# Performance work log

Hardware: AMD Instinct MI355X
Metric: run time of the kernel (lower is better)

Reference implementation:

```python
import jax, jax.numpy as jnp
import numpy as np

# Sizes (match input_specs)
B = 50                 # number of CRN graphs in the batch
NS_PER, NR_PER = 2000, 4000
N_S, N_R = B * NS_PER, B * NR_PER   # 100k species, 200k reactions total
E = 1_000_000          # bipartite edges
D = 128                # d_model
L = 2                  # n_layers
N_TYPES, P_DIM = 16, 8
MAX_SPECIES_IDX = 2000


def setup_inputs() -> dict:
    key = jax.random.key(0)
    ks = jax.random.split(key, 12)
    inp = {
        "species_indices": jax.random.randint(ks[0], (N_S,), 0, MAX_SPECIES_IDX, dtype=jnp.int32),
        "is_external": jax.random.randint(ks[1], (N_S,), 0, 2, dtype=jnp.int32),
        "propensity_type_ids": jax.random.randint(ks[2], (N_R,), 0, N_TYPES, dtype=jnp.int32),
        "propensity_params": jax.random.normal(ks[3], (N_R, P_DIM), dtype=jnp.float32),
        "edge_species": jax.random.randint(ks[4], (E,), 0, N_S, dtype=jnp.int32),
        "edge_reaction": jax.random.randint(ks[5], (E,), 0, N_R, dtype=jnp.int32),
        # contiguous per-graph segment ids (graphs are equal-sized)
        "species_batch": jnp.repeat(jnp.arange(B, dtype=jnp.int32), NS_PER),
        "reaction_batch": jnp.repeat(jnp.arange(B, dtype=jnp.int32), NR_PER),
        # learned parameters
        "species_table": jax.random.normal(ks[6], (MAX_SPECIES_IDX, D), dtype=jnp.float32) * 0.02,
        "external_table": jax.random.normal(ks[7], (2, D), dtype=jnp.float32) * 0.02,
        "type_table": jax.random.normal(ks[8], (N_TYPES, D), dtype=jnp.float32) * 0.02,
        "W_param": jax.random.normal(ks[9], (P_DIM, D), dtype=jnp.float32) * 0.1,
        "b_param": jnp.zeros((D,), dtype=jnp.float32),
        # per-layer message-passing weights: concat([h, msg]) -> d
        "Wr": jax.random.normal(ks[10], (L, 2 * D, D), dtype=jnp.float32) * 0.05,
        "br": jnp.zeros((L, D), dtype=jnp.float32),
        "Ws": jax.random.normal(ks[11], (L, 2 * D, D), dtype=jnp.float32) * 0.05,
        "bs": jnp.zeros((L, D), dtype=jnp.float32),
    }
    return inp


def reference(species_indices, is_external, propensity_type_ids, propensity_params,
              edge_species, edge_reaction, species_batch, reaction_batch,
              species_table, external_table, type_table, W_param, b_param,
              Wr, br, Ws, bs):
    # Initial embeddings
    h_s = species_table[species_indices] + external_table[is_external]          # (N_S, D)
    h_r = type_table[propensity_type_ids] + propensity_params @ W_param + b_param  # (N_R, D)

    n_s, n_r = h_s.shape[0], h_r.shape[0]
    # Alternating bipartite sum message passing (SumMessagePassingLayer)
    for l in range(Wr.shape[0]):
        m_r = jax.ops.segment_sum(h_s[edge_species], edge_reaction, num_segments=n_r)
        h_r = jax.nn.relu(jnp.concatenate([h_r, m_r], axis=-1) @ Wr[l] + br[l])
        m_s = jax.ops.segment_sum(h_r[edge_reaction], edge_species, num_segments=n_s)
        h_s = jax.nn.relu(jnp.concatenate([h_s, m_s], axis=-1) @ Ws[l] + bs[l])

    # Segment-mean pooling per graph (index_add then divide by counts)
    pooled_s = jax.ops.segment_sum(h_s, species_batch, num_segments=B) / float(NS_PER)
    pooled_r = jax.ops.segment_sum(h_r, reaction_batch, num_segments=B) / float(NR_PER)
    context = jnp.concatenate([pooled_s, pooled_r], axis=-1)  # (B, 2D); dropout p=0 -> identity
    return context
```

## Files before the change

### kernel.cpp

```cpp
#include <hip/hip_runtime.h>
#include <stdint.h>

#define NS 100000
#define NR 200000
#define EE 1000000
#define DD 128
#define NB 50
#define NSP 2000
#define NRP 4000
#define BSH 10
#define NBR 196
#define NBS 98
#define CHUNK 8192

typedef short bf16x8 __attribute__((ext_vector_type(8)));
typedef float f32x4 __attribute__((ext_vector_type(4)));
typedef unsigned u32x4 __attribute__((ext_vector_type(4)));
typedef unsigned u32x2 __attribute__((ext_vector_type(2)));

__device__ __forceinline__ unsigned short f2bf(float f){
  unsigned u = __float_as_uint(f);
  u = (u + 0x7FFFu + ((u >> 16) & 1u)) >> 16;
  return (unsigned short)u;
}
__device__ __forceinline__ float bf2f(unsigned short s){
  return __uint_as_float(((unsigned)s) << 16);
}
__device__ __forceinline__ unsigned packbf(float a, float b){
  return (unsigned)f2bf(a) | ((unsigned)f2bf(b) << 16);
}
__device__ __forceinline__ float bflo(unsigned p){ return __uint_as_float(p << 16); }
__device__ __forceinline__ float bfhi(unsigned p){ return __uint_as_float(p & 0xFFFF0000u); }

__global__ void pack_w(const float* __restrict__ Wr, const float* __restrict__ Ws,
                       unsigned short* __restrict__ Wp){
  int g = blockIdx.x*256 + threadIdx.x;
  if (g >= 4*32768) return;
  int j = g & 7; int rest = g >> 3;
  int lane = rest & 63; rest >>= 6;
  int ks = rest & 7; rest >>= 3;
  int ct = rest & 7; int mat = rest >> 3;
  int k  = ks*32 + (lane >> 4)*8 + j;
  int cc = ct*16 + (lane & 15);
  const float* src = (mat < 2) ? (Wr + (size_t)mat*256*DD) : (Ws + (size_t)(mat-2)*256*DD);
  Wp[g] = f2bf(src[(size_t)k*DD + cc]);
}

__global__ __launch_bounds__(256) void init_all(const int* __restrict__ si, const int* __restrict__ ext,
        const int* __restrict__ tid, const float* __restrict__ pp,
        const float* __restrict__ st, const float* __restrict__ et, const float* __restrict__ tt,
        const float* __restrict__ Wpar, const float* __restrict__ bpar,
        unsigned short* __restrict__ hs, unsigned short* __restrict__ hr){
  int g = blockIdx.x*256 + threadIdx.x;
  int row = g >> 4, colb = (g & 15) * 8;
  if (row < NS){
    const float* a = st + (size_t)si[row]*DD + colb;
    const float* b = et + (size_t)ext[row]*DD + colb;
    float4 x0 = ((const float4*)a)[0], x1 = ((const float4*)a)[1];
    float4 y0 = ((const float4*)b)[0], y1 = ((const float4*)b)[1];
    u32x4 o;
    o.x = packbf(x0.x+y0.x, x0.y+y0.y);
    o.y = packbf(x0.z+y0.z, x0.w+y0.w);
    o.z = packbf(x1.x+y1.x, x1.y+y1.y);
    o.w = packbf(x1.z+y1.z, x1.w+y1.w);
    *(u32x4*)(hs + (size_t)row*DD + colb) = o;
  } else {
    int r = row - NS;
    const float* tb = tt + (size_t)tid[r]*DD + colb;
    float4 a0 = ((const float4*)tb)[0], a1 = ((const float4*)tb)[1];
    float4 b0 = ((const float4*)(bpar+colb))[0], b1 = ((const float4*)(bpar+colb))[1];
    a0.x += b0.x; a0.y += b0.y; a0.z += b0.z; a0.w += b0.w;
    a1.x += b1.x; a1.y += b1.y; a1.z += b1.z; a1.w += b1.w;
    const float* pr = pp + (size_t)r*8;
    float4 p0 = ((const float4*)pr)[0], p1 = ((const float4*)pr)[1];
    float w[8] = {p0.x,p0.y,p0.z,p0.w,p1.x,p1.y,p1.z,p1.w};
    #pragma unroll
    for (int p = 0; p < 8; p++){
      float4 w0 = ((const float4*)(Wpar + p*DD + colb))[0];
      float4 w1 = ((const float4*)(Wpar + p*DD + colb))[1];
      a0.x += w[p]*w0.x; a0.y += w[p]*w0.y; a0.z += w[p]*w0.z; a0.w += w[p]*w0.w;
      a1.x += w[p]*w1.x; a1.y += w[p]*w1.y; a1.z += w[p]*w1.z; a1.w += w[p]*w1.w;
    }
    u32x4 o;
    o.x = packbf(a0.x, a0.y); o.y = packbf(a0.z, a0.w);
    o.z = packbf(a1.x, a1.y); o.w = packbf(a1.z, a1.w);
    *(u32x4*)(hr + (size_t)r*DD + colb) = o;
  }
}

__global__ __launch_bounds__(256) void bucket_hist(const int* __restrict__ er, const int* __restrict__ es,
                                                   int* __restrict__ gcnt){
  __shared__ int cnt[NBR + NBS];
  int t = threadIdx.x;
  for (int j = t; j < NBR + NBS; j += 256) cnt[j] = 0;
  __syncthreads();
  long i0 = (long)blockIdx.x * 2048;
  for (int j = t; j < 2048; j += 256){
    long i = i0 + j;
    if (i < EE){
      atomicAdd(&cnt[er[i] >> BSH], 1);
      atomicAdd(&cnt[NBR + (es[i] >> BSH)], 1);
    }
  }
  __syncthreads();
  for (int j = t; j < NBR + NBS; j += 256)
    if (cnt[j]) atomicAdd(&gcnt[j], cnt[j]);
}

__global__ __launch_bounds__(256) void bucket_scan(const int* __restrict__ gcnt,
        int* __restrict__ bktOffR, int* __restrict__ bktOffS,
        int* __restrict__ gCurR, int* __restrict__ gCurS){
  __shared__ int a[256];
  int t = threadIdx.x;
  int own = (t < NBR) ? gcnt[t] : 0;
  a[t] = own; __syncthreads();
  for (int d = 1; d < 256; d <<= 1){
    int x = (t >= d) ? a[t-d] : 0;
    __syncthreads(); a[t] += x; __syncthreads();
  }
  if (t < NBR){ int v = a[t] - own; bktOffR[t] = v; gCurR[t] = v; }
  if (t == 0) bktOffR[NBR] = EE;
  __syncthreads();
  own = (t < NBS) ? gcnt[NBR + t] : 0;
  a[t] = own; __syncthreads();
  for (int d = 1; d < 256; d <<= 1){
    int x = (t >= d) ? a[t-d] : 0;
    __syncthreads(); a[t] += x; __syncthreads();
  }
  if (t < NBS){ int v = a[t] - own; bktOffS[t] = v; gCurS[t] = v; }
  if (t == 0) bktOffS[NBS] = EE;
}

__global__ __launch_bounds__(256) void bin_edges(const int* __restrict__ er, const int* __restrict__ es,
        int* __restrict__ gCurR, int* __restrict__ gCurS,
        unsigned* __restrict__ recR, unsigned* __restrict__ recS){
  __shared__ unsigned stage[CHUNK];
  __shared__ unsigned char stageb[CHUNK];
  __shared__ int cnt[256], scn[256], pref[256], gbase[256], lcur[256];
  int t = threadIdx.x;
  int side = blockIdx.y;
  const int* dest = side ? es : er;
  const int* srca = side ? er : es;
  int* gCur = side ? gCurS : gCurR;
  unsigned* rec = side ? recS : recR;
  int nbkt = side ? NBS : NBR;
  long i0 = (long)blockIdx.x * CHUNK;
  int n = (EE - i0 < CHUNK) ? (int)(EE - i0) : CHUNK;
  cnt[t] = 0;
  __syncthreads();
  for (int j = t; j < n; j += 256)
    atomicAdd(&cnt[dest[i0 + j] >> BSH], 1);
  __syncthreads();
  scn[t] = cnt[t];
  __syncthreads();
  for (int d = 1; d < 256; d <<= 1){
    int x = (t >= d) ? scn[t-d] : 0;
    __syncthreads(); scn[t] += x; __syncthreads();
  }
  pref[t] = scn[t] - cnt[t];
  lcur[t] = scn[t] - cnt[t];
  if (t < nbkt && cnt[t] > 0) gbase[t] = atomicAdd(&gCur[t], cnt[t]);
  __syncthreads();
  for (int j = t; j < n; j += 256){
    int d = dest[i0 + j];
    int s = srca[i0 + j];
    int b = d >> BSH;
    int p = atomicAdd(&lcur[b], 1);
    stage[p] = ((unsigned)(d - (b << BSH)) << 18) | (unsigned)s;
    stageb[p] = (unsigned char)b;
  }
  __syncthreads();
  for (int e = t; e < n; e += 256){
    int b = stageb[e];
    rec[gbase[b] + (e - pref[b])] = stage[e];
  }
}

__global__ __launch_bounds__(256) void build_csr(const unsigned* __restrict__ recR, const unsigned* __restrict__ recS,
        const int* __restrict__ bktOffR, const int* __restrict__ bktOffS,
        unsigned* __restrict__ csrR, unsigned* __restrict__ csrS,
        int* __restrict__ offsR, int* __restrict__ offsS){
  __shared__ int hist[1024], pref[1024], cur[1024], ws[256];
  int t = threadIdx.x;
  int bb = blockIdx.x;
  const unsigned* rec; const int* bktOff; unsigned* csr; int* offs; int N;
  if (bb < NBR){ rec = recR; bktOff = bktOffR; csr = csrR; offs = offsR; N = NR; }
  else { bb -= NBR; rec = recS; bktOff = bktOffS; csr = csrS; offs = offsS; N = NS; }
  int d0 = bb << BSH;
  int base = bktOff[bb], cnt_ = bktOff[bb+1] - base;
  #pragma unroll
  for (int j = 0; j < 4; j++) hist[t*4+j] = 0;
  __syncthreads();
  for (int e = t; e < cnt_; e += 256)
    atomicAdd(&hist[rec[base + e] >> 18], 1);
  __syncthreads();
  int s = 0, h[4];
  #pragma unroll
  for (int j = 0; j < 4; j++){ h[j] = hist[t*4+j]; s += h[j]; }
  ws[t] = s;
  __syncthreads();
  for (int d = 1; d < 256; d <<= 1){
    int x = (t >= d) ? ws[t-d] : 0;
    __syncthreads(); ws[t] += x; __syncthreads();
  }
  int run = ws[t] - s;
  #pragma unroll
  for (int j = 0; j < 4; j++){ pref[t*4+j] = run; cur[t*4+j] = base + run; run += h[j]; }
  __syncthreads();
  int DPB = N - d0; if (DPB > 1024) DPB = 1024;
  #pragma unroll
  for (int j = 0; j < 4; j++){
    int i = t*4 + j;
    if (i < DPB) offs[d0 + i] = base + pref[i];
  }
  if (t == 0 && d0 + DPB == N) offs[N] = EE;
  __syncthreads();
  for (int e = t; e < cnt_; e += 256){
    unsigned r = rec[base + e];
    int pos = atomicAdd(&cur[r >> 18], 1);
    csr[pos] = r;
  }
}

__global__ __launch_bounds__(256) void fused_layer(
        const unsigned short* __restrict__ gsrc,
        const unsigned short* __restrict__ hself,
        const int* __restrict__ offs, const unsigned* __restrict__ csr,
        const unsigned short* __restrict__ Wp, const float* __restrict__ bias,
        unsigned short* __restrict__ hout)
{
  __shared__ unsigned short msgT[32*DD];
  int t = threadIdx.x;
  int lane = t & 63;
  int w = t >> 6;
  int quad = lane >> 4, rlo = lane & 15;
  int row0 = blockIdx.x * 32;

  for (int i = t; i < 2048; i += 256) ((unsigned*)msgT)[i] = 0u;
  __syncthreads();

  {
    int rbeg = row0 + w*8;
    int k  = offs[rbeg];
    int ke = offs[rbeg + 8];
    int c16 = lane >> 2, sub4 = lane & 3;
    float a0 = 0.f, a1 = 0.f;
    int cur = -1;
    unsigned rc[4]; unsigned pv[4];
    if (k < ke){
      #pragma unroll
      for (int i = 0; i < 4; i++){
        int kk = (k + i < ke) ? (k + i) : (ke - 1);
        rc[i] = csr[kk];
      }
      #pragma unroll
      for (int i = 0; i < 4; i++)
        pv[i] = *(const unsigned*)(gsrc + (size_t)(rc[i] & 0x3FFFF)*DD + lane*2);
      while (k < ke){
        unsigned rc2[4], pv2[4];
        int kn = k + 4;
        #pragma unroll
        for (int i = 0; i < 4; i++){
          int kk = (kn + i < ke) ? (kn + i) : (ke - 1);
          rc2[i] = csr[kk];
        }
        #pragma unroll
        for (int i = 0; i < 4; i++)
          pv2[i] = *(const unsigned*)(gsrc + (size_t)(rc2[i] & 0x3FFFF)*DD + lane*2);
        #pragma unroll
        for (int i = 0; i < 4; i++){
          if (k + i < ke){
            int dl = (int)((rc[i] >> 18) & 31);
            if (dl != cur){
              if (cur >= 0)
                *(unsigned*)(msgT + cur*DD + ((c16 ^ (cur & 7)) << 3) + (sub4 << 1)) = packbf(a0, a1);
              a0 = 0.f; a1 = 0.f;
              cur = dl;
            }
            a0 += bflo(pv[i]); a1 += bfhi(pv[i]);
          }
        }
        #pragma unroll
        for (int i = 0; i < 4; i++){ rc[i] = rc2[i]; pv[i] = pv2[i]; }
        k = kn;
      }
      if (cur >= 0)
        *(unsigned*)(msgT + cur*DD + ((c16 ^ (cur & 7)) << 3) + (sub4 << 1)) = packbf(a0, a1);
    }
  }
  __syncthreads();

  int ct0 = w * 2;
  bf16x8 wf[16];
  #pragma unroll
  for (int ks = 0; ks < 8; ks++){
    wf[ks*2+0] = *(const bf16x8*)(Wp + (size_t)(((ct0+0)*8 + ks)*64 + lane) * 8);
    wf[ks*2+1] = *(const bf16x8*)(Wp + (size_t)(((ct0+1)*8 + ks)*64 + lane) * 8);
  }
  bf16x8 Hb0[4], Hb1[4];
  #pragma unroll
  for (int ks = 0; ks < 4; ks++){
    int kloc = ks*32 + quad*8;
    Hb0[ks] = *(const bf16x8*)(hself + (size_t)(row0 + rlo) * DD + kloc);
    Hb1[ks] = *(const bf16x8*)(hself + (size_t)(row0 + 16 + rlo) * DD + kloc);
  }
  bf16x8 Mb0[4], Mb1[4];
  #pragma unroll
  for (int ks2 = 0; ks2 < 4; ks2++){
    int c8 = ks2*4 + quad;
    int lr0 = rlo, lr1 = 16 + rlo;
    Mb0[ks2] = *(const bf16x8*)(msgT + lr0*DD + ((c8 ^ (lr0 & 7)) * 8));
    Mb1[ks2] = *(const bf16x8*)(msgT + lr1*DD + ((c8 ^ (lr1 & 7)) * 8));
  }

  f32x4 acc[2][2];
  #pragma unroll
  for (int i = 0; i < 2; i++)
    #pragma unroll
    for (int j = 0; j < 2; j++){ f32x4 z = {0.f,0.f,0.f,0.f}; acc[i][j] = z; }

  #pragma unroll
  for (int ks = 0; ks < 4; ks++){
    acc[0][0] = __builtin_amdgcn_mfma_f32_16x16x32_bf16(wf[ks*2+0], Hb0[ks], acc[0][0], 0, 0, 0);
    acc[0][1] = __builtin_amdgcn_mfma_f32_16x16x32_bf16(wf[ks*2+1], Hb0[ks], acc[0][1], 0, 0, 0);
    acc[1][0] = __builtin_amdgcn_mfma_f32_16x16x32_bf16(wf[ks*2+0], Hb1[ks], acc[1][0], 0, 0, 0);
    acc[1][1] = __builtin_amdgcn_mfma_f32_16x16x32_bf16(wf[ks*2+1], Hb1[ks], acc[1][1], 0, 0, 0);
  }
  #pragma unroll
  for (int ks2 = 0; ks2 < 4; ks2++){
    int ks = 4 + ks2;
    acc[0][0] = __builtin_amdgcn_mfma_f32_16x16x32_bf16(wf[ks*2+0], Mb0[ks2], acc[0][0], 0, 0, 0);
    acc[0][1] = __builtin_amdgcn_mfma_f32_16x16x32_bf16(wf[ks*2+1], Mb0[ks2], acc[0][1], 0, 0, 0);
    acc[1][0] = __builtin_amdgcn_mfma_f32_16x16x32_bf16(wf[ks*2+0], Mb1[ks2], acc[1][0], 0, 0, 0);
    acc[1][1] = __builtin_amdgcn_mfma_f32_16x16x32_bf16(wf[ks*2+1], Mb1[ks2], acc[1][1], 0, 0, 0);
  }

  #pragma unroll
  for (int c = 0; c < 2; c++){
    float4 bv = *(const float4*)(bias + (ct0+c)*16 + quad*4);
    #pragma unroll
    for (int rb = 0; rb < 2; rb++){
      int row = row0 + rb*16 + rlo;
      float v0 = acc[rb][c][0] + bv.x;
      float v1 = acc[rb][c][1] + bv.y;
      float v2 = acc[rb][c][2] + bv.z;
      float v3 = acc[rb][c][3] + bv.w;
      v0 = v0 > 0.f ? v0 : 0.f;
      v1 = v1 > 0.f ? v1 : 0.f;
      v2 = v2 > 0.f ? v2 : 0.f;
      v3 = v3 > 0.f ? v3 : 0.f;
      u32x2 o; o.x = packbf(v0, v1); o.y = packbf(v2, v3);
      *(u32x2*)(hout + (size_t)row*DD + (ct0+c)*16 + quad*4) = o;
    }
  }
}

__global__ __launch_bounds__(256) void pool(const unsigned short* __restrict__ hs,
        const unsigned short* __restrict__ hr, float* __restrict__ out){
  __shared__ float red[16][128];
  int b = blockIdx.x, part = blockIdx.y;
  int t = threadIdx.x;
  int rg = t >> 4, sub = t & 15;
  const unsigned short* src; int row0, outoff; float scale;
  if (part < 4){ src = hs; row0 = b*NSP + part*500; outoff = b*256; scale = 1.f/NSP; }
  else { src = hr; row0 = b*NRP + (part-4)*500; outoff = b*256 + 128; scale = 1.f/NRP; }
  float a0=0,a1=0,a2=0,a3=0,a4=0,a5=0,a6=0,a7=0;
  for (int r = rg; r < 500; r += 16){
    u32x4 p = *(const u32x4*)(src + (size_t)(row0+r)*DD + sub*8);
    a0 += bflo(p.x); a1 += bfhi(p.x);
    a2 += bflo(p.y); a3 += bfhi(p.y);
    a4 += bflo(p.z); a5 += bfhi(p.z);
    a6 += bflo(p.w); a7 += bfhi(p.w);
  }
  float* rr = &red[rg][sub*8];
  rr[0]=a0; rr[1]=a1; rr[2]=a2; rr[3]=a3; rr[4]=a4; rr[5]=a5; rr[6]=a6; rr[7]=a7;
  __syncthreads();
  if (t < 128){
    float s = 0.f;
    #pragma unroll
    for (int g = 0; g < 16; g++) s += red[g][t];
    atomicAdd(&out[outoff + t], s * scale);
  }
}

extern "C" void kernel_launch(void* const* d_in, const int* in_sizes, int n_in,
                              void* d_out, int out_size, void* d_ws, size_t ws_size,
                              hipStream_t stream)
{
  const int*   si   = (const int*)d_in[0];
  const int*   ext  = (const int*)d_in[1];
  const int*   tid  = (const int*)d_in[2];
  const float* pp   = (const float*)d_in[3];
  const int*   es   = (const int*)d_in[4];
  const int*   er   = (const int*)d_in[5];
  const float* st   = (const float*)d_in[8];
  const float* et   = (const float*)d_in[9];
  const float* tt   = (const float*)d_in[10];
  const float* Wpar = (const float*)d_in[11];
  const float* bpar = (const float*)d_in[12];
  const float* Wr   = (const float*)d_in[13];
  const float* br   = (const float*)d_in[14];
  const float* Ws   = (const float*)d_in[15];
  const float* bs   = (const float*)d_in[16];
  float* out = (float*)d_out;

  char* basep = (char*)d_ws; size_t off = 0;
  auto alloc = [&](size_t bytes)->char*{
    char* r = basep + off; off = (off + bytes + 255) & ~(size_t)255; return r;
  };
  unsigned short* hs0 = (unsigned short*)alloc((size_t)NS*DD*2);
  unsigned short* hs1 = (unsigned short*)alloc((size_t)NS*DD*2);
  unsigned short* hr0 = (unsigned short*)alloc((size_t)NR*DD*2);
  unsigned short* hr1 = (unsigned short*)alloc((size_t)NR*DD*2);
  unsigned short* Wp  = (unsigned short*)alloc((size_t)4*32768*2);
  int* offsR = (int*)alloc((size_t)(NR+1)*4);
  int* offsS = (int*)alloc((size_t)(NS+1)*4);
  unsigned* csrR = (unsigned*)alloc((size_t)EE*4);
  unsigned* csrS = (unsigned*)alloc((size_t)EE*4);
  int* gcnt   = (int*)alloc(2048);
  int* bktOffR= (int*)alloc(2048);
  int* bktOffS= (int*)alloc(2048);
  int* gCurR  = (int*)alloc(2048);
  int* gCurS  = (int*)alloc(2048);
  unsigned* recR = (unsigned*)hs1;
  unsigned* recS = (unsigned*)hr1;

  hipMemsetAsync(gcnt, 0, 2048, stream);
  hipMemsetAsync(d_out, 0, (size_t)out_size*4, stream);

  pack_w<<<512, 256, 0, stream>>>(Wr, Ws, Wp);
  init_all<<<(NS+NR)*16/256, 256, 0, stream>>>(si, ext, tid, pp, st, et, tt, Wpar, bpar, hs0, hr0);

  bucket_hist<<<(EE + 2047)/2048, 256, 0, stream>>>(er, es, gcnt);
  bucket_scan<<<1, 256, 0, stream>>>(gcnt, bktOffR, bktOffS, gCurR, gCurS);
  bin_edges<<<dim3((EE + CHUNK - 1)/CHUNK, 2), 256, 0, stream>>>(er, es, gCurR, gCurS, recR, recS);
  build_csr<<<NBR + NBS, 256, 0, stream>>>(recR, recS, bktOffR, bktOffS, csrR, csrS, offsR, offsS);

  fused_layer<<<NR/32, 256, 0, stream>>>(hs0, hr0, offsR, csrR, Wp + (size_t)0*32768, br + (size_t)0*DD, hr1);
  fused_layer<<<NS/32, 256, 0, stream>>>(hr1, hs0, offsS, csrS, Wp + (size_t)2*32768, bs + (size_t)0*DD, hs1);
  fused_layer<<<NR/32, 256, 0, stream>>>(hs1, hr1, offsR, csrR, Wp + (size_t)1*32768, br + (size_t)1*DD, hr0);
  fused_layer<<<NS/32, 256, 0, stream>>>(hr0, hs1, offsS, csrS, Wp + (size_t)3*32768, bs + (size_t)1*DD, hs0);

  pool<<<dim3(NB, 12), 256, 0, stream>>>(hs0, hr0, out);
}
```

Baseline: 506.1 us.

## Gather neighbor features from FP8 shadow copies in message passing

Adds FP8 shadow copies of the species and reaction embeddings, written by the init kernel and by each fused layer next to the bf16 output. The edge-gather phase now reads 1-byte FP8 values per feature instead of bf16, halving the random-gather traffic that dominates the message-passing kernels. The cost is extra FP8 writes per layer and lower precision in the summed messages, which may hurt accuracy against the fp32 reference.

```diff
diff --git a/kernel.cpp b/kernel.cpp
--- a/kernel.cpp
+++ b/kernel.cpp
@@ -15,6 +15,7 @@
 
 typedef short bf16x8 __attribute__((ext_vector_type(8)));
 typedef float f32x4 __attribute__((ext_vector_type(4)));
+typedef float f32x2 __attribute__((ext_vector_type(2)));
 typedef unsigned u32x4 __attribute__((ext_vector_type(4)));
 typedef unsigned u32x2 __attribute__((ext_vector_type(2)));
 
@@ -31,6 +32,15 @@
 }
 __device__ __forceinline__ float bflo(unsigned p){ return __uint_as_float(p << 16); }
 __device__ __forceinline__ float bfhi(unsigned p){ return __uint_as_float(p & 0xFFFF0000u); }
+
+__device__ __forceinline__ u32x2 packf8(const float* v){
+  u32x2 r;
+  unsigned w = __builtin_amdgcn_cvt_pk_fp8_f32(v[0], v[1], 0u, false);
+  r.x = __builtin_amdgcn_cvt_pk_fp8_f32(v[2], v[3], w, true);
+  w = __builtin_amdgcn_cvt_pk_fp8_f32(v[4], v[5], 0u, false);
+  r.y = __builtin_amdgcn_cvt_pk_fp8_f32(v[6], v[7], w, true);
+  return r;
+}
 
 __global__ void pack_w(const float* __restrict__ Wr, const float* __restrict__ Ws,
                        unsigned short* __restrict__ Wp){
@@ -50,20 +60,23 @@
         const int* __restrict__ tid, const float* __restrict__ pp,
         const float* __restrict__ st, const float* __restrict__ et, const float* __restrict__ tt,
         const float* __restrict__ Wpar, const float* __restrict__ bpar,
-        unsigned short* __restrict__ hs, unsigned short* __restrict__ hr){
+        unsigned short* __restrict__ hs, unsigned short* __restrict__ hr,
+        unsigned char* __restrict__ f8S, unsigned char* __restrict__ f8R){
   int g = blockIdx.x*256 + threadIdx.x;
   int row = g >> 4, colb = (g & 15) * 8;
+  float v[8];
   if (row < NS){
     const float* a = st + (size_t)si[row]*DD + colb;
     const float* b = et + (size_t)ext[row]*DD + colb;
     float4 x0 = ((const float4*)a)[0], x1 = ((const float4*)a)[1];
     float4 y0 = ((const float4*)b)[0], y1 = ((const float4*)b)[1];
+    v[0]=x0.x+y0.x; v[1]=x0.y+y0.y; v[2]=x0.z+y0.z; v[3]=x0.w+y0.w;
+    v[4]=x1.x+y1.x; v[5]=x1.y+y1.y; v[6]=x1.z+y1.z; v[7]=x1.w+y1.w;
     u32x4 o;
-    o.x = packbf(x0.x+y0.x, x0.y+y0.y);
-    o.y = packbf(x0.z+y0.z, x0.w+y0.w);
-    o.z = packbf(x1.x+y1.x, x1.y+y1.y);
-    o.w = packbf(x1.z+y1.z, x1.w+y1.w);
+    o.x = packbf(v[0],v[1]); o.y = packbf(v[2],v[3]);
+    o.z = packbf(v[4],v[5]); o.w = packbf(v[6],v[7]);
     *(u32x4*)(hs + (size_t)row*DD + colb) = o;
+    *(u32x2*)(f8S + (size_t)row*DD + colb) = packf8(v);
   } else {
     int r = row - NS;
     const float* tb = tt + (size_t)tid[r]*DD + colb;
@@ -81,10 +94,13 @@
       a0.x += w[p]*w0.x; a0.y += w[p]*w0.y; a0.z += w[p]*w0.z; a0.w += w[p]*w0.w;
       a1.x += w[p]*w1.x; a1.y += w[p]*w1.y; a1.z += w[p]*w1.z; a1.w += w[p]*w1.w;
     }
+    v[0]=a0.x; v[1]=a0.y; v[2]=a0.z; v[3]=a0.w;
+    v[4]=a1.x; v[5]=a1.y; v[6]=a1.z; v[7]=a1.w;
     u32x4 o;
-    o.x = packbf(a0.x, a0.y); o.y = packbf(a0.z, a0.w);
-    o.z = packbf(a1.x, a1.y); o.w = packbf(a1.z, a1.w);
+    o.x = packbf(v[0],v[1]); o.y = packbf(v[2],v[3]);
+    o.z = packbf(v[4],v[5]); o.w = packbf(v[6],v[7]);
     *(u32x4*)(hr + (size_t)r*DD + colb) = o;
+    *(u32x2*)(f8R + (size_t)r*DD + colb) = packf8(v);
   }
 }
 
@@ -223,11 +239,11 @@
 }
 
 __global__ __launch_bounds__(256) void fused_layer(
-        const unsigned short* __restrict__ gsrc,
+        const unsigned char* __restrict__ g8,
         const unsigned short* __restrict__ hself,
         const int* __restrict__ offs, const unsigned* __restrict__ csr,
         const unsigned short* __restrict__ Wp, const float* __restrict__ bias,
-        unsigned short* __restrict__ hout)
+        unsigned short* __restrict__ hout, unsigned char* __restrict__ hout8)
 {
   __shared__ unsigned short msgT[32*DD];
   int t = threadIdx.x;
@@ -246,7 +262,7 @@
     int c16 = lane >> 2, sub4 = lane & 3;
     float a0 = 0.f, a1 = 0.f;
     int cur = -1;
-    unsigned rc[4]; unsigned pv[4];
+    unsigned rc[4]; unsigned short pv[4];
     if (k < ke){
       #pragma unroll
       for (int i = 0; i < 4; i++){
@@ -255,9 +271,9 @@
       }
       #pragma unroll
       for (int i = 0; i < 4; i++)
-        pv[i] = *(const unsigned*)(gsrc + (size_t)(rc[i] & 0x3FFFF)*DD + lane*2);
+        pv[i] = *(const unsigned short*)(g8 + (size_t)(rc[i] & 0x3FFFF)*DD + lane*2);
       while (k < ke){
-        unsigned rc2[4], pv2[4];
+        unsigned rc2[4]; unsigned short pv2[4];
         int kn = k + 4;
         #pragma unroll
         for (int i = 0; i < 4; i++){
@@ -266,7 +282,7 @@
         }
         #pragma unroll
         for (int i = 0; i < 4; i++)
-          pv2[i] = *(const unsigned*)(gsrc + (size_t)(rc2[i] & 0x3FFFF)*DD + lane*2);
+          pv2[i] = *(const unsigned short*)(g8 + (size_t)(rc2[i] & 0x3FFFF)*DD + lane*2);
         #pragma unroll
         for (int i = 0; i < 4; i++){
           if (k + i < ke){
@@ -277,7 +293,8 @@
               a0 = 0.f; a1 = 0.f;
               cur = dl;
             }
-            a0 += bflo(pv[i]); a1 += bfhi(pv[i]);
+            f32x2 f = __builtin_amdgcn_cvt_pk_f32_fp8((unsigned)pv[i], false);
+            a0 += f.x; a1 += f.y;
           }
         }
         #pragma unroll
@@ -351,6 +368,9 @@
       v3 = v3 > 0.f ? v3 : 0.f;
       u32x2 o; o.x = packbf(v0, v1); o.y = packbf(v2, v3);
       *(u32x2*)(hout + (size_t)row*DD + (ct0+c)*16 + quad*4) = o;
+      unsigned w8 = __builtin_amdgcn_cvt_pk_fp8_f32(v0, v1, 0u, false);
+      w8 = __builtin_amdgcn_cvt_pk_fp8_f32(v2, v3, w8, true);
+      *(unsigned*)(hout8 + (size_t)row*DD + (ct0+c)*16 + quad*4) = w8;
     }
   }
 }
@@ -412,6 +432,8 @@
   unsigned short* hs1 = (unsigned short*)alloc((size_t)NS*DD*2);
   unsigned short* hr0 = (unsigned short*)alloc((size_t)NR*DD*2);
   unsigned short* hr1 = (unsigned short*)alloc((size_t)NR*DD*2);
+  unsigned char*  f8S = (unsigned char*)alloc((size_t)NS*DD);
+  unsigned char*  f8R = (unsigned char*)alloc((size_t)NR*DD);
   unsigned short* Wp  = (unsigned short*)alloc((size_t)4*32768*2);
   int* offsR = (int*)alloc((size_t)(NR+1)*4);
   int* offsS = (int*)alloc((size_t)(NS+1)*4);
@@ -429,17 +451,18 @@
   hipMemsetAsync(d_out, 0, (size_t)out_size*4, stream);
 
   pack_w<<<512, 256, 0, stream>>>(Wr, Ws, Wp);
-  init_all<<<(NS+NR)*16/256, 256, 0, stream>>>(si, ext, tid, pp, st, et, tt, Wpar, bpar, hs0, hr0);
+  init_all<<<(NS+NR)*16/256, 256, 0, stream>>>(si, ext, tid, pp, st, et, tt, Wpar, bpar,
+                                               hs0, hr0, f8S, f8R);
 
   bucket_hist<<<(EE + 2047)/2048, 256, 0, stream>>>(er, es, gcnt);
   bucket_scan<<<1, 256, 0, stream>>>(gcnt, bktOffR, bktOffS, gCurR, gCurS);
   bin_edges<<<dim3((EE + CHUNK - 1)/CHUNK, 2), 256, 0, stream>>>(er, es, gCurR, gCurS, recR, recS);
   build_csr<<<NBR + NBS, 256, 0, stream>>>(recR, recS, bktOffR, bktOffS, csrR, csrS, offsR, offsS);
 
-  fused_layer<<<NR/32, 256, 0, stream>>>(hs0, hr0, offsR, csrR, Wp + (size_t)0*32768, br + (size_t)0*DD, hr1);
-  fused_layer<<<NS/32, 256, 0, stream>>>(hr1, hs0, offsS, csrS, Wp + (size_t)2*32768, bs + (size_t)0*DD, hs1);
-  fused_layer<<<NR/32, 256, 0, stream>>>(hs1, hr1, offsR, csrR, Wp + (size_t)1*32768, br + (size_t)1*DD, hr0);
-  fused_layer<<<NS/32, 256, 0, stream>>>(hr0, hs1, offsS, csrS, Wp + (size_t)3*32768, bs + (size_t)1*DD, hs0);
+  fused_layer<<<NR/32, 256, 0, stream>>>(f8S, hr0, offsR, csrR, Wp + (size_t)0*32768, br + (size_t)0*DD, hr1, f8R);
+  fused_layer<<<NS/32, 256, 0, stream>>>(f8R, hs0, offsS, csrS, Wp + (size_t)2*32768, bs + (size_t)0*DD, hs1, f8S);
+  fused_layer<<<NR/32, 256, 0, stream>>>(f8S, hr1, offsR, csrR, Wp + (size_t)1*32768, br + (size_t)1*DD, hr0, f8R);
+  fused_layer<<<NS/32, 256, 0, stream>>>(f8R, hs1, offsS, csrS, Wp + (size_t)3*32768, bs + (size_t)1*DD, hs0, f8S);
 
   pool<<<dim3(NB, 12), 256, 0, stream>>>(hs0, hr0, out);
 }
```

After: 542.5 us. 1.07x slower.
